# Optimization experiments

Measured on AMD Instinct MI355X. Metric: run time of the kernel, lower is better.

Reference implementation:

```python
import jax, jax.numpy as jnp
import numpy as np

N_NODES = 50000
N_EDGES = 800000
IN_DIM = 128
HID = 64
N_GRAPHS = 256


def setup_inputs() -> dict:
    key = jax.random.key(0)
    ks = jax.random.split(key, 10)
    s = lambda d: 1.0 / np.sqrt(d)
    return {
        'x': jax.random.normal(ks[0], (N_NODES, IN_DIM), jnp.float32),
        'edge_index': jax.random.randint(ks[1], (2, N_EDGES), 0, N_NODES, jnp.int64),
        'batch': jnp.sort(jax.random.randint(ks[2], (N_NODES,), 0, N_GRAPHS, jnp.int64)),
        'Wp': jax.random.normal(ks[3], (IN_DIM, HID), jnp.float32) * s(IN_DIM),
        'bp': jnp.zeros((HID,), jnp.float32),
        'W1_0': jax.random.normal(ks[4], (HID, HID), jnp.float32) * s(HID),
        'b1_0': jnp.zeros((HID,), jnp.float32),
        'W2_0': jax.random.normal(ks[5], (HID, HID), jnp.float32) * s(HID),
        'b2_0': jnp.zeros((HID,), jnp.float32),
        'W1_1': jax.random.normal(ks[6], (HID, HID), jnp.float32) * s(HID),
        'b1_1': jnp.zeros((HID,), jnp.float32),
        'W2_1': jax.random.normal(ks[7], (HID, HID), jnp.float32) * s(HID),
        'b2_1': jnp.zeros((HID,), jnp.float32),
    }


def _gin_layer(h, src, dst, W1, b1, W2, b2):
    # scatter-add aggregation: sum_{j in N(i)} h_j  (messages flow src -> dst)
    agg = jax.ops.segment_sum(h[src], dst, num_segments=N_NODES)
    z = h + agg  # eps = 0 (GINConv default)
    z = jax.nn.relu(z @ W1 + b1)
    z = z @ W2 + b2
    return jax.nn.relu(z)  # outer activation from SharedGINEncoder


def reference(x, edge_index, batch, Wp, bp, W1_0, b1_0, W2_0, b2_0, W1_1, b1_1, W2_1, b2_1):
    src, dst = edge_index[0], edge_index[1]
    h = jax.nn.relu(x @ Wp + bp)  # [N, HID]
    h = _gin_layer(h, src, dst, W1_0, b1_0, W2_0, b2_0)
    h = _gin_layer(h, src, dst, W1_1, b1_1, W2_1, b2_1)
    # global_mean_pool over graph ids
    sums = jax.ops.segment_sum(h, batch, num_segments=N_GRAPHS)  # [G, HID]
    counts = jax.ops.segment_sum(jnp.ones((h.shape[0],), h.dtype), batch, num_segments=N_GRAPHS)
    return sums / jnp.maximum(counts, 1.0)[:, None]
```

## Files before the change

kernel.cpp:

```cpp
#include <hip/hip_runtime.h>

#define N_NODES 50000
#define N_EDGES 800000
#define IN_DIM 128
#define HID 64
#define N_GRAPHS 256

#define E_PER_BLK 4000
#define F_BLOCKS (N_EDGES / E_PER_BLK)
#define NBKT ((N_NODES + 255) / 256)
#define CNT_N (NBKT * F_BLOCKS)
#define SCB ((CNT_N + 255) / 256)
#define NTILES (N_NODES / 4)
#define MTILES (N_NODES / 16)
#define DCNT_N (64 * NBKT)
#define DSCB ((DCNT_N + 255) / 256)


__device__ __forceinline__ float bf2f(unsigned short v) {
  return __uint_as_float(((unsigned int)v) << 16);
}
__device__ __forceinline__ unsigned short f2bf(float f) {
  unsigned int u = __float_as_uint(f);
  return (unsigned short)((u + 0x7fffu + ((u >> 16) & 1u)) >> 16);
}

typedef __attribute__((ext_vector_type(8))) short bf16x8;
typedef __attribute__((ext_vector_type(4))) float f32x4;

__global__ __launch_bounds__(256) void part_hist_kernel(const int* __restrict__ dst,
                                                        int* __restrict__ cnt) {
  __shared__ int h[NBKT];
  const int t = threadIdx.x;
  for (int k = t; k < NBKT; k += 256) h[k] = 0;
  __syncthreads();
  const int base = blockIdx.x * E_PER_BLK;
  for (int i = t; i < E_PER_BLK; i += 256) atomicAdd(&h[dst[base + i] >> 8], 1);
  __syncthreads();
  for (int k = t; k < NBKT; k += 256) cnt[k * F_BLOCKS + blockIdx.x] = h[k];
}

__global__ __launch_bounds__(256) void scan1g_kernel(const int* __restrict__ in,
                                                     int* __restrict__ ex,
                                                     int* __restrict__ bsum, int n) {
  __shared__ int s[256];
  const int t = threadIdx.x;
  const int i = blockIdx.x * 256 + t;
  int v = (i < n) ? in[i] : 0;
  s[t] = v;
  __syncthreads();
#pragma unroll
  for (int ofs = 1; ofs < 256; ofs <<= 1) {
    int u = (t >= ofs) ? s[t - ofs] : 0;
    __syncthreads();
    s[t] += u;
    __syncthreads();
  }
  if (i < n) ex[i] = s[t] - v;
  if (t == 255) bsum[blockIdx.x] = s[255];
}

__global__ __launch_bounds__(256) void scan2g_kernel(const int* __restrict__ bsum,
                                                     int* __restrict__ bpref, int nb) {
  __shared__ int s[256];
  const int t = threadIdx.x;
  int v = (t < nb) ? bsum[t] : 0;
  s[t] = v;
  __syncthreads();
#pragma unroll
  for (int ofs = 1; ofs < 256; ofs <<= 1) {
    int u = (t >= ofs) ? s[t - ofs] : 0;
    __syncthreads();
    s[t] += u;
    __syncthreads();
  }
  if (t < nb) bpref[t] = s[t] - v;
}

__global__ __launch_bounds__(256) void part_scatter_kernel(const int* __restrict__ src,
                                                           const int* __restrict__ dst,
                                                           const int* __restrict__ cex,
                                                           const int* __restrict__ bpref,
                                                           int* __restrict__ psrc,
                                                           int* __restrict__ pdst) {
  __shared__ int cur[NBKT];
  const int t = threadIdx.x;
  for (int k = t; k < NBKT; k += 256) {
    const int i = k * F_BLOCKS + blockIdx.x;
    cur[k] = cex[i] + bpref[i >> 8];
  }
  __syncthreads();
  const int base = blockIdx.x * E_PER_BLK;
  for (int i = t; i < E_PER_BLK; i += 256) {
    int d = dst[base + i], s = src[base + i];
    int p = atomicAdd(&cur[d >> 8], 1);
    pdst[p] = d;
    psrc[p] = s;
  }
}

__global__ __launch_bounds__(256) void bucket_sort_kernel(const int* __restrict__ psrc,
                                                          const int* __restrict__ pdst,
                                                          const int* __restrict__ cex,
                                                          const int* __restrict__ bpref,
                                                          int* __restrict__ csr,
                                                          int* __restrict__ off,
                                                          int* __restrict__ dcnt) {
  const int k = blockIdx.x;
  const int t = threadIdx.x;
  const int i0 = k * F_BLOCKS;
  const int b0 = cex[i0] + bpref[i0 >> 8];
  int b1 = N_EDGES;
  if (k != NBKT - 1) {
    const int i1 = (k + 1) * F_BLOCKS;
    b1 = cex[i1] + bpref[i1 >> 8];
  }
  __shared__ int cnt[256];
  __shared__ int s[256];
  __shared__ int cur[256];
  __shared__ int dhist[64];
  cnt[t] = 0;
  if (t < 64) dhist[t] = 0;
  __syncthreads();
  for (int i = b0 + t; i < b1; i += 256) atomicAdd(&cnt[pdst[i] & 255], 1);
  __syncthreads();
  int v = cnt[t];
  s[t] = v;
  __syncthreads();
#pragma unroll
  for (int ofs = 1; ofs < 256; ofs <<= 1) {
    int u = (t >= ofs) ? s[t - ofs] : 0;
    __syncthreads();
    s[t] += u;
    __syncthreads();
  }
  const int node = (k << 8) + t;
  const int start = b0 + s[t] - v;
  cur[t] = start;
  if (node < N_NODES) {
    off[node] = start;
    atomicAdd(&dhist[(v < 63) ? v : 63], 1);
  }
  if (k == NBKT - 1 && t == 0) off[N_NODES] = N_EDGES;
  __syncthreads();
  if (t < 64) dcnt[t * NBKT + k] = dhist[t];
  for (int i = b0 + t; i < b1; i += 256) {
    int d = pdst[i];
    int p = atomicAdd(&cur[d & 255], 1);
    csr[p] = psrc[i];
  }
}

__global__ __launch_bounds__(256) void perm_scatter_kernel(const int* __restrict__ off,
                                                           const int* __restrict__ dex,
                                                           const int* __restrict__ dbpref,
                                                           int* __restrict__ perm) {
  __shared__ int cur[64];
  const int k = blockIdx.x, t = threadIdx.x;
  if (t < 64) {
    const int i = t * NBKT + k;
    cur[t] = dex[i] + dbpref[i >> 8];
  }
  __syncthreads();
  const int node = (k << 8) + t;
  if (node < N_NODES) {
    int d = off[node + 1] - off[node];
    d = (d < 63) ? d : 63;
    int pos = atomicAdd(&cur[d], 1);
    perm[pos] = node;
  }
}

__global__ __launch_bounds__(256) void proj_kernel(
    const float* __restrict__ x, const float* __restrict__ Wp,
    const float* __restrict__ bp, unsigned short* __restrict__ h) {
  __shared__ __align__(16) float sX[2][2][4][64];
  __shared__ __align__(16) float sPart[2][2][4][64];
  const int wave = threadIdx.x >> 6, lane = threadIdx.x & 63;
  const int pair = wave >> 1, khalf = wave & 1;
  float w[64];
#pragma unroll
  for (int k = 0; k < 64; ++k) w[k] = Wp[(khalf * 64 + k) * HID + lane];
  const float bias = bp[lane];
  const int pv = blockIdx.x * 2 + pair;
  const int np = gridDim.x * 2;
  const int iters = (NTILES - blockIdx.x * 2 + np - 1) / np;
  for (int it = 0; it < iters; ++it) {
    const int tile = pv + it * np;
    const bool act = (tile < NTILES);
    const int n0 = tile * 4;
    const int buf = it & 1;
    if (act) {
#pragma unroll
      for (int t = 0; t < 4; ++t)
        sX[pair][khalf][t][lane] = x[(n0 + t) * IN_DIM + khalf * 64 + lane];
    }
    float p[4];
#pragma unroll
    for (int t = 0; t < 4; ++t) {
      float a0 = khalf ? 0.f : bias, a1 = 0.f, a2 = 0.f, a3 = 0.f;
#pragma unroll
      for (int k = 0; k < 64; k += 4) {
        float4 v = *(const float4*)&sX[pair][khalf][t][k];
        a0 = fmaf(v.x, w[k + 0], a0);
        a1 = fmaf(v.y, w[k + 1], a1);
        a2 = fmaf(v.z, w[k + 2], a2);
        a3 = fmaf(v.w, w[k + 3], a3);
      }
      p[t] = (a0 + a1) + (a2 + a3);
    }
    if (act && khalf) {
#pragma unroll
      for (int t = 0; t < 4; ++t) sPart[pair][buf][t][lane] = p[t];
    }
    __syncthreads();
    if (act && !khalf) {
#pragma unroll
      for (int t = 0; t < 4; ++t)
        h[(n0 + t) * HID + lane] = f2bf(fmaxf(p[t] + sPart[pair][buf][t][lane], 0.0f));
    }
  }
}

__global__ __launch_bounds__(256) void gin_fused_mfma_kernel(
    const unsigned short* __restrict__ h_in, const int* __restrict__ off,
    const int* __restrict__ csr, const int* __restrict__ perm,
    const float* __restrict__ W1, const float* __restrict__ b1,
    const float* __restrict__ W2, const float* __restrict__ b2,
    unsigned short* __restrict__ h_out) {
  __shared__ __align__(16) unsigned short sW1[4096];
  __shared__ __align__(16) unsigned short sW2[4096];
  __shared__ __align__(16) unsigned short sT[4][16][72];
  const int t = threadIdx.x;
  for (int i = t; i < 4096; i += 256) {
    const int k = i >> 6, j = i & 63;
    const int pos = (((j >> 4) * 2 + (k >> 5)) * 64 + ((k >> 3) & 3) * 16 + (j & 15)) * 8 + (k & 7);
    sW1[pos] = f2bf(W1[i]);
    sW2[pos] = f2bf(W2[i]);
  }
  __syncthreads();
  const int wave = t >> 6, lane = t & 63;
  const int row = lane & 15;
  const int kgrp = lane >> 4;
  float bias1[4], bias2[4];
#pragma unroll
  for (int nc = 0; nc < 4; ++nc) {
    bias1[nc] = b1[nc * 16 + row];
    bias2[nc] = b2[nc * 16 + row];
  }
  const uint4* __restrict__ hv = (const uint4*)h_in;
  const int tile = blockIdx.x * 4 + wave;
  if (tile < MTILES) {
    const int n = perm[(tile << 4) + row];
    const int o0 = off[n];
    const int deg = off[n + 1] - o0;
    int dm = deg;
#pragma unroll
    for (int m = 1; m <= 8; m <<= 1) {
      int o = __shfl_xor(dm, m);
      dm = (o > dm) ? o : dm;
    }
    float ac0[8], ac1[8];
    {
      uint4 ua = hv[n * 8 + kgrp];
      uint4 ub = hv[n * 8 + 4 + kgrp];
      const unsigned int* pa = (const unsigned int*)&ua;
      const unsigned int* pb = (const unsigned int*)&ub;
#pragma unroll
      for (int e = 0; e < 4; ++e) {
        ac0[2 * e] = bf2f((unsigned short)(pa[e] & 0xffff));
        ac0[2 * e + 1] = bf2f((unsigned short)(pa[e] >> 16));
        ac1[2 * e] = bf2f((unsigned short)(pb[e] & 0xffff));
        ac1[2 * e + 1] = bf2f((unsigned short)(pb[e] >> 16));
      }
    }
    for (int j = 0; j < dm; j += 4) {
#pragma unroll
      for (int u = 0; u < 4; ++u) {
        const int jj = j + u;
        const int pos = o0 + ((jj < deg) ? jj : 0);
        const int idx = csr[(pos < N_EDGES) ? pos : (N_EDGES - 1)];
        const float m = (jj < deg) ? 1.0f : 0.0f;
        uint4 ua = hv[idx * 8 + kgrp];
        uint4 ub = hv[idx * 8 + 4 + kgrp];
        const unsigned int* pa = (const unsigned int*)&ua;
        const unsigned int* pb = (const unsigned int*)&ub;
#pragma unroll
        for (int e = 0; e < 4; ++e) {
          ac0[2 * e] = fmaf(m, bf2f((unsigned short)(pa[e] & 0xffff)), ac0[2 * e]);
          ac0[2 * e + 1] = fmaf(m, bf2f((unsigned short)(pa[e] >> 16)), ac0[2 * e + 1]);
          ac1[2 * e] = fmaf(m, bf2f((unsigned short)(pb[e] & 0xffff)), ac1[2 * e]);
          ac1[2 * e + 1] = fmaf(m, bf2f((unsigned short)(pb[e] >> 16)), ac1[2 * e + 1]);
        }
      }
    }
    bf16x8 a1[2];
#pragma unroll
    for (int e = 0; e < 8; ++e) {
      a1[0][e] = (short)f2bf(ac0[e]);
      a1[1][e] = (short)f2bf(ac1[e]);
    }
    f32x4 acc;
#pragma unroll
    for (int nc = 0; nc < 4; ++nc) {
      acc = (f32x4){bias1[nc], bias1[nc], bias1[nc], bias1[nc]};
#pragma unroll
      for (int ks = 0; ks < 2; ++ks) {
        bf16x8 bf = *(const bf16x8*)&sW1[((nc * 2 + ks) * 64 + lane) * 8];
        acc = __builtin_amdgcn_mfma_f32_16x16x32_bf16(a1[ks], bf, acc, 0, 0, 0);
      }
#pragma unroll
      for (int r = 0; r < 4; ++r)
        sT[wave][kgrp * 4 + r][nc * 16 + row] = f2bf(fmaxf(acc[r], 0.0f));
    }
    bf16x8 a2[2];
    a2[0] = *(const bf16x8*)&sT[wave][row][kgrp * 8];
    a2[1] = *(const bf16x8*)&sT[wave][row][32 + kgrp * 8];
#pragma unroll
    for (int nc = 0; nc < 4; ++nc) {
      acc = (f32x4){bias2[nc], bias2[nc], bias2[nc], bias2[nc]};
#pragma unroll
      for (int ks = 0; ks < 2; ++ks) {
        bf16x8 bf = *(const bf16x8*)&sW2[((nc * 2 + ks) * 64 + lane) * 8];
        acc = __builtin_amdgcn_mfma_f32_16x16x32_bf16(a2[ks], bf, acc, 0, 0, 0);
      }
#pragma unroll
      for (int r = 0; r < 4; ++r)
        sT[wave][kgrp * 4 + r][nc * 16 + row] = f2bf(fmaxf(acc[r], 0.0f));
    }
#pragma unroll
    for (int p = 0; p < 2; ++p) {
      const int idx2 = p * 64 + lane;
      const int ri = idx2 >> 3, ch = idx2 & 7;
      const int nodeo = perm[(tile << 4) + ri];
      uint4 v = *(const uint4*)&sT[wave][ri][ch * 8];
      *(uint4*)&h_out[nodeo * HID + ch * 8] = v;
    }
  }
}

__global__ __launch_bounds__(256) void pool_kernel(const unsigned short* __restrict__ h,
                                                   const int* __restrict__ batch,
                                                   float* __restrict__ out) {
  const int g = blockIdx.x;
  int lo = 0, hi = N_NODES;
  while (lo < hi) {
    int mid = (lo + hi) >> 1;
    if (batch[mid] < g) lo = mid + 1; else hi = mid;
  }
  const int s = lo;
  hi = N_NODES;
  while (lo < hi) {
    int mid = (lo + hi) >> 1;
    if (batch[mid] < g + 1) lo = mid + 1; else hi = mid;
  }
  const int e = lo;
  const int wave = threadIdx.x >> 6, lane = threadIdx.x & 63;
  float a0 = 0.f, a1 = 0.f, a2 = 0.f, a3 = 0.f;
  int n = s + wave;
  for (; n + 12 < e; n += 16) {
    a0 += bf2f(h[n * HID + lane]);
    a1 += bf2f(h[(n + 4) * HID + lane]);
    a2 += bf2f(h[(n + 8) * HID + lane]);
    a3 += bf2f(h[(n + 12) * HID + lane]);
  }
  for (; n < e; n += 4) a0 += bf2f(h[n * HID + lane]);
  __shared__ float red[4][HID];
  red[wave][lane] = ((a0 + a1) + (a2 + a3));
  __syncthreads();
  if (wave == 0) {
    float v = red[0][lane] + red[1][lane] + red[2][lane] + red[3][lane];
    float cnt = (float)(e - s);
    out[g * HID + lane] = v / fmaxf(cnt, 1.0f);
  }
}

extern "C" void kernel_launch(void* const* d_in, const int* in_sizes, int n_in,
                              void* d_out, int out_size, void* d_ws, size_t ws_size,
                              hipStream_t stream) {
  const float* x    = (const float*)d_in[0];
  const int*   edge = (const int*)d_in[1];
  const int*   batch= (const int*)d_in[2];
  const float* Wp   = (const float*)d_in[3];
  const float* bp   = (const float*)d_in[4];
  const float* W1_0 = (const float*)d_in[5];
  const float* b1_0 = (const float*)d_in[6];
  const float* W2_0 = (const float*)d_in[7];
  const float* b2_0 = (const float*)d_in[8];
  const float* W1_1 = (const float*)d_in[9];
  const float* b1_1 = (const float*)d_in[10];
  const float* W2_1 = (const float*)d_in[11];
  const float* b2_1 = (const float*)d_in[12];
  const int* src = edge;
  const int* dst = edge + N_EDGES;
  float* out = (float*)d_out;

  const size_t NB = (size_t)N_NODES * HID;
  unsigned short* hA = (unsigned short*)d_ws;
  unsigned short* hB = hA + NB;
  int* off     = (int*)(hB + NB);
  int* cnt     = off + N_NODES + 1;
  int* cex     = cnt + CNT_N;
  int* sbsum   = cex + CNT_N;
  int* sbpref  = sbsum + SCB;
  int* dcnt    = sbpref + SCB;
  int* dex     = dcnt + DCNT_N;
  int* dbsum   = dex + DCNT_N;
  int* dbpref  = dbsum + DSCB;
  int* perm    = dbpref + DSCB;
  int* pdst    = perm + N_NODES;
  int* psrc    = pdst + N_EDGES;
  int* csr     = psrc + N_EDGES;

  dim3 b256(256);

  part_hist_kernel<<<F_BLOCKS, b256, 0, stream>>>(dst, cnt);
  scan1g_kernel<<<SCB, b256, 0, stream>>>(cnt, cex, sbsum, CNT_N);
  scan2g_kernel<<<1, b256, 0, stream>>>(sbsum, sbpref, SCB);
  part_scatter_kernel<<<F_BLOCKS, b256, 0, stream>>>(src, dst, cex, sbpref, psrc, pdst);
  bucket_sort_kernel<<<NBKT, b256, 0, stream>>>(psrc, pdst, cex, sbpref, csr, off, dcnt);

  scan1g_kernel<<<DSCB, b256, 0, stream>>>(dcnt, dex, dbsum, DCNT_N);
  scan2g_kernel<<<1, b256, 0, stream>>>(dbsum, dbpref, DSCB);
  perm_scatter_kernel<<<NBKT, b256, 0, stream>>>(off, dex, dbpref, perm);

  proj_kernel<<<2048, b256, 0, stream>>>(x, Wp, bp, hA);

  gin_fused_mfma_kernel<<<782, b256, 0, stream>>>(hA, off, csr, perm, W1_0, b1_0, W2_0, b2_0, hB);
  gin_fused_mfma_kernel<<<782, b256, 0, stream>>>(hB, off, csr, perm, W1_1, b1_1, W2_1, b2_1, hA);

  pool_kernel<<<N_GRAPHS, b256, 0, stream>>>(hA, batch, out);
}
```

Baseline: 133.2 us.

## Split each GIN tile's neighbor gather across two waves and combine partials

Each 16-node tile is now handled by a pair of waves in 512-thread blocks. Each wave gathers half of every node's neighbor list, and the partial sums are exchanged through shared memory. Each wave then computes half of the output columns of both MLP matmuls. This roughly halves the serial gather latency per wave and doubles the waves in flight. In exchange it adds three block-wide barriers, extra LDS traffic, and an extra bf16 rounding of the partial sums.

```diff
diff --git a/kernel.cpp b/kernel.cpp
--- a/kernel.cpp
+++ b/kernel.cpp
@@ -222,7 +222,7 @@
   }
 }
 
-__global__ __launch_bounds__(256) void gin_fused_mfma_kernel(
+__global__ __launch_bounds__(512) void gin_fused_mfma_kernel(
     const unsigned short* __restrict__ h_in, const int* __restrict__ off,
     const int* __restrict__ csr, const int* __restrict__ perm,
     const float* __restrict__ W1, const float* __restrict__ b1,
@@ -230,9 +230,11 @@
     unsigned short* __restrict__ h_out) {
   __shared__ __align__(16) unsigned short sW1[4096];
   __shared__ __align__(16) unsigned short sW2[4096];
-  __shared__ __align__(16) unsigned short sT[4][16][72];
-  const int t = threadIdx.x;
-  for (int i = t; i < 4096; i += 256) {
+  __shared__ __align__(16) unsigned short sPar[2][4][16][72];
+  __shared__ __align__(16) unsigned short sT1[4][16][72];
+  __shared__ __align__(16) unsigned short sT2[4][16][72];
+  const int t = threadIdx.x;
+  for (int i = t; i < 4096; i += 512) {
     const int k = i >> 6, j = i & 63;
     const int pos = (((j >> 4) * 2 + (k >> 5)) * 64 + ((k >> 3) & 3) * 16 + (j & 15)) * 8 + (k & 7);
     sW1[pos] = f2bf(W1[i]);
@@ -240,102 +242,127 @@
   }
   __syncthreads();
   const int wave = t >> 6, lane = t & 63;
+  const int pair = wave >> 1, half = wave & 1;
   const int row = lane & 15;
   const int kgrp = lane >> 4;
-  float bias1[4], bias2[4];
-#pragma unroll
-  for (int nc = 0; nc < 4; ++nc) {
-    bias1[nc] = b1[nc * 16 + row];
-    bias2[nc] = b2[nc * 16 + row];
+  const int tile = blockIdx.x * 4 + pair;
+  const bool act = (tile < MTILES);
+  int n = 0, o0 = 0, deg = 0;
+  if (act) {
+    n = perm[(tile << 4) + row];
+    o0 = off[n];
+    deg = off[n + 1] - o0;
+  }
+  const int jbeg = half ? (deg + 1) >> 1 : 0;
+  const int jend = half ? deg : (deg + 1) >> 1;
+  const int cntw = jend - jbeg;
+  int dm = cntw;
+#pragma unroll
+  for (int m = 1; m <= 8; m <<= 1) {
+    int o = __shfl_xor(dm, m);
+    dm = (o > dm) ? o : dm;
   }
   const uint4* __restrict__ hv = (const uint4*)h_in;
-  const int tile = blockIdx.x * 4 + wave;
-  if (tile < MTILES) {
-    const int n = perm[(tile << 4) + row];
-    const int o0 = off[n];
-    const int deg = off[n + 1] - o0;
-    int dm = deg;
-#pragma unroll
-    for (int m = 1; m <= 8; m <<= 1) {
-      int o = __shfl_xor(dm, m);
-      dm = (o > dm) ? o : dm;
-    }
-    float ac0[8], ac1[8];
-    {
-      uint4 ua = hv[n * 8 + kgrp];
-      uint4 ub = hv[n * 8 + 4 + kgrp];
+  float ac0[8], ac1[8];
+#pragma unroll
+  for (int e = 0; e < 8; ++e) {
+    ac0[e] = 0.0f;
+    ac1[e] = 0.0f;
+  }
+  if (act && !half) {
+    uint4 ua = hv[n * 8 + kgrp];
+    uint4 ub = hv[n * 8 + 4 + kgrp];
+    const unsigned int* pa = (const unsigned int*)&ua;
+    const unsigned int* pb = (const unsigned int*)&ub;
+#pragma unroll
+    for (int e = 0; e < 4; ++e) {
+      ac0[2 * e] = bf2f((unsigned short)(pa[e] & 0xffff));
+      ac0[2 * e + 1] = bf2f((unsigned short)(pa[e] >> 16));
+      ac1[2 * e] = bf2f((unsigned short)(pb[e] & 0xffff));
+      ac1[2 * e + 1] = bf2f((unsigned short)(pb[e] >> 16));
+    }
+  }
+  for (int j = 0; j < dm; j += 4) {
+#pragma unroll
+    for (int u = 0; u < 4; ++u) {
+      const int jj = j + u;
+      int pos = o0 + jbeg + ((jj < cntw) ? jj : 0);
+      const int idx = csr[(pos < N_EDGES) ? pos : (N_EDGES - 1)];
+      const float m = (jj < cntw) ? 1.0f : 0.0f;
+      uint4 ua = hv[idx * 8 + kgrp];
+      uint4 ub = hv[idx * 8 + 4 + kgrp];
       const unsigned int* pa = (const unsigned int*)&ua;
       const unsigned int* pb = (const unsigned int*)&ub;
 #pragma unroll
       for (int e = 0; e < 4; ++e) {
-        ac0[2 * e] = bf2f((unsigned short)(pa[e] & 0xffff));
-        ac0[2 * e + 1] = bf2f((unsigned short)(pa[e] >> 16));
-        ac1[2 * e] = bf2f((unsigned short)(pb[e] & 0xffff));
-        ac1[2 * e + 1] = bf2f((unsigned short)(pb[e] >> 16));
+        ac0[2 * e] = fmaf(m, bf2f((unsigned short)(pa[e] & 0xffff)), ac0[2 * e]);
+        ac0[2 * e + 1] = fmaf(m, bf2f((unsigned short)(pa[e] >> 16)), ac0[2 * e + 1]);
+        ac1[2 * e] = fmaf(m, bf2f((unsigned short)(pb[e] & 0xffff)), ac1[2 * e]);
+        ac1[2 * e + 1] = fmaf(m, bf2f((unsigned short)(pb[e] >> 16)), ac1[2 * e + 1]);
       }
     }
-    for (int j = 0; j < dm; j += 4) {
-#pragma unroll
-      for (int u = 0; u < 4; ++u) {
-        const int jj = j + u;
-        const int pos = o0 + ((jj < deg) ? jj : 0);
-        const int idx = csr[(pos < N_EDGES) ? pos : (N_EDGES - 1)];
-        const float m = (jj < deg) ? 1.0f : 0.0f;
-        uint4 ua = hv[idx * 8 + kgrp];
-        uint4 ub = hv[idx * 8 + 4 + kgrp];
-        const unsigned int* pa = (const unsigned int*)&ua;
-        const unsigned int* pb = (const unsigned int*)&ub;
-#pragma unroll
-        for (int e = 0; e < 4; ++e) {
-          ac0[2 * e] = fmaf(m, bf2f((unsigned short)(pa[e] & 0xffff)), ac0[2 * e]);
-          ac0[2 * e + 1] = fmaf(m, bf2f((unsigned short)(pa[e] >> 16)), ac0[2 * e + 1]);
-          ac1[2 * e] = fmaf(m, bf2f((unsigned short)(pb[e] & 0xffff)), ac1[2 * e]);
-          ac1[2 * e + 1] = fmaf(m, bf2f((unsigned short)(pb[e] >> 16)), ac1[2 * e + 1]);
-        }
-      }
-    }
-    bf16x8 a1[2];
+  }
+  {
+    bf16x8 p0, p1;
 #pragma unroll
     for (int e = 0; e < 8; ++e) {
-      a1[0][e] = (short)f2bf(ac0[e]);
-      a1[1][e] = (short)f2bf(ac1[e]);
-    }
-    f32x4 acc;
-#pragma unroll
-    for (int nc = 0; nc < 4; ++nc) {
-      acc = (f32x4){bias1[nc], bias1[nc], bias1[nc], bias1[nc]};
-#pragma unroll
-      for (int ks = 0; ks < 2; ++ks) {
-        bf16x8 bf = *(const bf16x8*)&sW1[((nc * 2 + ks) * 64 + lane) * 8];
-        acc = __builtin_amdgcn_mfma_f32_16x16x32_bf16(a1[ks], bf, acc, 0, 0, 0);
-      }
-#pragma unroll
-      for (int r = 0; r < 4; ++r)
-        sT[wave][kgrp * 4 + r][nc * 16 + row] = f2bf(fmaxf(acc[r], 0.0f));
-    }
-    bf16x8 a2[2];
-    a2[0] = *(const bf16x8*)&sT[wave][row][kgrp * 8];
-    a2[1] = *(const bf16x8*)&sT[wave][row][32 + kgrp * 8];
-#pragma unroll
-    for (int nc = 0; nc < 4; ++nc) {
-      acc = (f32x4){bias2[nc], bias2[nc], bias2[nc], bias2[nc]};
-#pragma unroll
-      for (int ks = 0; ks < 2; ++ks) {
-        bf16x8 bf = *(const bf16x8*)&sW2[((nc * 2 + ks) * 64 + lane) * 8];
-        acc = __builtin_amdgcn_mfma_f32_16x16x32_bf16(a2[ks], bf, acc, 0, 0, 0);
-      }
-#pragma unroll
-      for (int r = 0; r < 4; ++r)
-        sT[wave][kgrp * 4 + r][nc * 16 + row] = f2bf(fmaxf(acc[r], 0.0f));
-    }
-#pragma unroll
-    for (int p = 0; p < 2; ++p) {
-      const int idx2 = p * 64 + lane;
-      const int ri = idx2 >> 3, ch = idx2 & 7;
-      const int nodeo = perm[(tile << 4) + ri];
-      uint4 v = *(const uint4*)&sT[wave][ri][ch * 8];
-      *(uint4*)&h_out[nodeo * HID + ch * 8] = v;
-    }
+      p0[e] = (short)f2bf(ac0[e]);
+      p1[e] = (short)f2bf(ac1[e]);
+    }
+    *(bf16x8*)&sPar[half][pair][row][kgrp * 8] = p0;
+    *(bf16x8*)&sPar[half][pair][row][32 + kgrp * 8] = p1;
+  }
+  __syncthreads();
+  bf16x8 a1[2];
+  {
+    bf16x8 q0 = *(const bf16x8*)&sPar[1 - half][pair][row][kgrp * 8];
+    bf16x8 q1 = *(const bf16x8*)&sPar[1 - half][pair][row][32 + kgrp * 8];
+#pragma unroll
+    for (int e = 0; e < 8; ++e) {
+      a1[0][e] = (short)f2bf(ac0[e] + bf2f((unsigned short)q0[e]));
+      a1[1][e] = (short)f2bf(ac1[e] + bf2f((unsigned short)q1[e]));
+    }
+  }
+  f32x4 acc;
+#pragma unroll
+  for (int q = 0; q < 2; ++q) {
+    const int nc = 2 * half + q;
+    const float bb = b1[nc * 16 + row];
+    acc = (f32x4){bb, bb, bb, bb};
+#pragma unroll
+    for (int ks = 0; ks < 2; ++ks) {
+      bf16x8 bf = *(const bf16x8*)&sW1[((nc * 2 + ks) * 64 + lane) * 8];
+      acc = __builtin_amdgcn_mfma_f32_16x16x32_bf16(a1[ks], bf, acc, 0, 0, 0);
+    }
+#pragma unroll
+    for (int r = 0; r < 4; ++r)
+      sT1[pair][kgrp * 4 + r][nc * 16 + row] = f2bf(fmaxf(acc[r], 0.0f));
+  }
+  __syncthreads();
+  bf16x8 a2[2];
+  a2[0] = *(const bf16x8*)&sT1[pair][row][kgrp * 8];
+  a2[1] = *(const bf16x8*)&sT1[pair][row][32 + kgrp * 8];
+#pragma unroll
+  for (int q = 0; q < 2; ++q) {
+    const int nc = 2 * half + q;
+    const float bb = b2[nc * 16 + row];
+    acc = (f32x4){bb, bb, bb, bb};
+#pragma unroll
+    for (int ks = 0; ks < 2; ++ks) {
+      bf16x8 bf = *(const bf16x8*)&sW2[((nc * 2 + ks) * 64 + lane) * 8];
+      acc = __builtin_amdgcn_mfma_f32_16x16x32_bf16(a2[ks], bf, acc, 0, 0, 0);
+    }
+#pragma unroll
+    for (int r = 0; r < 4; ++r)
+      sT2[pair][kgrp * 4 + r][nc * 16 + row] = f2bf(fmaxf(acc[r], 0.0f));
+  }
+  __syncthreads();
+  if (act) {
+    const int idx2 = half * 64 + lane;
+    const int ri = idx2 >> 3, ch = idx2 & 7;
+    const int nodeo = perm[(tile << 4) + ri];
+    uint4 v = *(const uint4*)&sT2[pair][ri][ch * 8];
+    *(uint4*)&h_out[nodeo * HID + ch * 8] = v;
   }
 }
 
@@ -412,7 +439,7 @@
   int* psrc    = pdst + N_EDGES;
   int* csr     = psrc + N_EDGES;
 
-  dim3 b256(256);
+  dim3 b256(256), b512(512);
 
   part_hist_kernel<<<F_BLOCKS, b256, 0, stream>>>(dst, cnt);
   scan1g_kernel<<<SCB, b256, 0, stream>>>(cnt, cex, sbsum, CNT_N);
@@ -426,8 +453,8 @@
 
   proj_kernel<<<2048, b256, 0, stream>>>(x, Wp, bp, hA);
 
-  gin_fused_mfma_kernel<<<782, b256, 0, stream>>>(hA, off, csr, perm, W1_0, b1_0, W2_0, b2_0, hB);
-  gin_fused_mfma_kernel<<<782, b256, 0, stream>>>(hB, off, csr, perm, W1_1, b1_1, W2_1, b2_1, hA);
+  gin_fused_mfma_kernel<<<782, b512, 0, stream>>>(hA, off, csr, perm, W1_0, b1_0, W2_0, b2_0, hB);
+  gin_fused_mfma_kernel<<<782, b512, 0, stream>>>(hB, off, csr, perm, W1_1, b1_1, W2_1, b2_1, hA);
 
   pool_kernel<<<N_GRAPHS, b256, 0, stream>>>(hA, batch, out);
 }
```

Result: slower. 142.0 us (+6.6%).

## Rewrite input projection as bf16 MFMA kernel with swizzled LDS weights

Applied to the files above, without the earlier changes.

Replaces the scalar FMA projection kernel (fp32 weights in registers, two waves splitting K and reducing through shared memory) with an MFMA 16x16x32 bf16 kernel. Each wave handles a 16-node tile, converts x to bf16 on load, keeps Wp pre-swizzled in LDS, and writes output through an LDS transpose for coalesced 16-byte stores. This aims to cut the projection's compute and sync cost, which matters most if that stage is compute-bound rather than bound by reading x. The cost is bf16 rounding of x and Wp, plus the per-block Wp conversion into LDS.

```diff
diff --git a/kernel.cpp b/kernel.cpp
--- a/kernel.cpp
+++ b/kernel.cpp
@@ -11,7 +11,6 @@
 #define NBKT ((N_NODES + 255) / 256)
 #define CNT_N (NBKT * F_BLOCKS)
 #define SCB ((CNT_N + 255) / 256)
-#define NTILES (N_NODES / 4)
 #define MTILES (N_NODES / 16)
 #define DCNT_N (64 * NBKT)
 #define DSCB ((DCNT_N + 255) / 256)
@@ -171,53 +170,61 @@
   }
 }
 
-__global__ __launch_bounds__(256) void proj_kernel(
+__global__ __launch_bounds__(256) void proj_mfma_kernel(
     const float* __restrict__ x, const float* __restrict__ Wp,
     const float* __restrict__ bp, unsigned short* __restrict__ h) {
-  __shared__ __align__(16) float sX[2][2][4][64];
-  __shared__ __align__(16) float sPart[2][2][4][64];
-  const int wave = threadIdx.x >> 6, lane = threadIdx.x & 63;
-  const int pair = wave >> 1, khalf = wave & 1;
-  float w[64];
-#pragma unroll
-  for (int k = 0; k < 64; ++k) w[k] = Wp[(khalf * 64 + k) * HID + lane];
-  const float bias = bp[lane];
-  const int pv = blockIdx.x * 2 + pair;
-  const int np = gridDim.x * 2;
-  const int iters = (NTILES - blockIdx.x * 2 + np - 1) / np;
-  for (int it = 0; it < iters; ++it) {
-    const int tile = pv + it * np;
-    const bool act = (tile < NTILES);
-    const int n0 = tile * 4;
-    const int buf = it & 1;
-    if (act) {
-#pragma unroll
-      for (int t = 0; t < 4; ++t)
-        sX[pair][khalf][t][lane] = x[(n0 + t) * IN_DIM + khalf * 64 + lane];
-    }
-    float p[4];
-#pragma unroll
-    for (int t = 0; t < 4; ++t) {
-      float a0 = khalf ? 0.f : bias, a1 = 0.f, a2 = 0.f, a3 = 0.f;
-#pragma unroll
-      for (int k = 0; k < 64; k += 4) {
-        float4 v = *(const float4*)&sX[pair][khalf][t][k];
-        a0 = fmaf(v.x, w[k + 0], a0);
-        a1 = fmaf(v.y, w[k + 1], a1);
-        a2 = fmaf(v.z, w[k + 2], a2);
-        a3 = fmaf(v.w, w[k + 3], a3);
+  __shared__ __align__(16) unsigned short sWp[8192];
+  __shared__ __align__(16) unsigned short sT[4][16][72];
+  const int t = threadIdx.x;
+  for (int i = t; i < 8192; i += 256) {
+    const int k = i >> 6, j = i & 63;
+    const int pos = (((j >> 4) * 4 + (k >> 5)) * 64 + ((k >> 3) & 3) * 16 + (j & 15)) * 8 + (k & 7);
+    sWp[pos] = f2bf(Wp[i]);
+  }
+  __syncthreads();
+  const int wave = t >> 6, lane = t & 63;
+  const int row = lane & 15;
+  const int kgrp = lane >> 4;
+  float bias[4];
+#pragma unroll
+  for (int nc = 0; nc < 4; ++nc) bias[nc] = bp[nc * 16 + row];
+  const int tile = blockIdx.x * 4 + wave;
+  if (tile < MTILES) {
+    const int n = tile * 16 + row;
+    bf16x8 a[4];
+#pragma unroll
+    for (int ks = 0; ks < 4; ++ks) {
+      float4 v0 = *(const float4*)&x[n * IN_DIM + ks * 32 + kgrp * 8];
+      float4 v1 = *(const float4*)&x[n * IN_DIM + ks * 32 + kgrp * 8 + 4];
+      a[ks][0] = (short)f2bf(v0.x);
+      a[ks][1] = (short)f2bf(v0.y);
+      a[ks][2] = (short)f2bf(v0.z);
+      a[ks][3] = (short)f2bf(v0.w);
+      a[ks][4] = (short)f2bf(v1.x);
+      a[ks][5] = (short)f2bf(v1.y);
+      a[ks][6] = (short)f2bf(v1.z);
+      a[ks][7] = (short)f2bf(v1.w);
+    }
+    f32x4 acc;
+#pragma unroll
+    for (int nc = 0; nc < 4; ++nc) {
+      acc = (f32x4){bias[nc], bias[nc], bias[nc], bias[nc]};
+#pragma unroll
+      for (int ks = 0; ks < 4; ++ks) {
+        bf16x8 bf = *(const bf16x8*)&sWp[((nc * 4 + ks) * 64 + lane) * 8];
+        acc = __builtin_amdgcn_mfma_f32_16x16x32_bf16(a[ks], bf, acc, 0, 0, 0);
       }
-      p[t] = (a0 + a1) + (a2 + a3);
-    }
-    if (act && khalf) {
-#pragma unroll
-      for (int t = 0; t < 4; ++t) sPart[pair][buf][t][lane] = p[t];
-    }
-    __syncthreads();
-    if (act && !khalf) {
-#pragma unroll
-      for (int t = 0; t < 4; ++t)
-        h[(n0 + t) * HID + lane] = f2bf(fmaxf(p[t] + sPart[pair][buf][t][lane], 0.0f));
+#pragma unroll
+      for (int r = 0; r < 4; ++r)
+        sT[wave][kgrp * 4 + r][nc * 16 + row] = f2bf(fmaxf(acc[r], 0.0f));
+    }
+    const int n0 = tile * 16;
+#pragma unroll
+    for (int p = 0; p < 2; ++p) {
+      const int idx2 = p * 64 + lane;
+      const int ri = idx2 >> 3, ch = idx2 & 7;
+      uint4 v = *(const uint4*)&sT[wave][ri][ch * 8];
+      *(uint4*)&h[(n0 + ri) * HID + ch * 8] = v;
     }
   }
 }
@@ -424,7 +431,7 @@
   scan2g_kernel<<<1, b256, 0, stream>>>(dbsum, dbpref, DSCB);
   perm_scatter_kernel<<<NBKT, b256, 0, stream>>>(off, dex, dbpref, perm);
 
-  proj_kernel<<<2048, b256, 0, stream>>>(x, Wp, bp, hA);
+  proj_mfma_kernel<<<782, b256, 0, stream>>>(x, Wp, bp, hA);
 
   gin_fused_mfma_kernel<<<782, b256, 0, stream>>>(hA, off, csr, perm, W1_0, b1_0, W2_0, b2_0, hB);
   gin_fused_mfma_kernel<<<782, b256, 0, stream>>>(hB, off, csr, perm, W1_1, b1_1, W2_1, b2_1, hA);
```

Result: faster. 127.6 us (-4.2%).
